# Optimization experiments

Measured on AMD Instinct MI355X. Metric: run time of the kernel, lower is better.

Reference implementation:

```python
import jax, jax.numpy as jnp
import numpy as np

HIDDEN = 128

def setup_inputs() -> dict:
    key = jax.random.key(0)
    k1, k2, k3, k4, k5, k6 = jax.random.split(key, 6)
    n_nodes, n_edges, h = 100000, 500000, HIDDEN
    node_features_after_gcn = jax.random.normal(k1, (n_nodes, h), dtype=jnp.float32)
    edges = jax.random.randint(k2, (2, n_edges), 0, n_nodes, dtype=jnp.int64)
    # edge_classifier params: Linear(2h -> 4h), Linear(4h -> 2)
    W1 = jax.random.normal(k3, (2 * h, 4 * h), dtype=jnp.float32) / np.sqrt(2 * h)
    b1 = jax.random.normal(k4, (4 * h,), dtype=jnp.float32) * 0.01
    W2 = jax.random.normal(k5, (4 * h, 2), dtype=jnp.float32) / np.sqrt(4 * h)
    b2 = jax.random.normal(k6, (2,), dtype=jnp.float32) * 0.01
    return {"node_features_after_gcn": node_features_after_gcn, "edges": edges,
            "W1": W1, "b1": b1, "W2": W2, "b2": b2}

def reference(node_features_after_gcn, W1, b1, W2, b2, edges):
    # gather endpoint features: [E, h] each (node1/node2 projections are Identity)
    first = node_features_after_gcn[edges[0], :]
    second = node_features_after_gcn[edges[1], :]
    edge_feat = jnp.concatenate((first, second), axis=1)  # [E, 2h]
    edge_feat = jax.nn.relu(edge_feat)
    hidden = jax.nn.relu(edge_feat @ W1 + b1)  # [E, 4h]
    return hidden @ W2 + b2  # [E, 2]
```

## Files before the change

### kernel.cpp

```cpp
#include <hip/hip_runtime.h>
#include <stdint.h>

#define HID  128
#define N1   512
#define NCAT 1024
#define NTB  48

typedef _Float16 f16;
typedef __attribute__((ext_vector_type(8))) _Float16 f16x8;
typedef __attribute__((ext_vector_type(4))) _Float16 f16x4;
typedef __attribute__((ext_vector_type(2))) _Float16 f16x2;
typedef __attribute__((ext_vector_type(8))) short   short8;
typedef __attribute__((ext_vector_type(4))) float   floatx4;
typedef __attribute__((ext_vector_type(2))) float   floatx2;
typedef __attribute__((ext_vector_type(8))) __bf16  bf16x8;

static __device__ __forceinline__ short f2bf(float x) {
  uint32_t u = __builtin_bit_cast(uint32_t, x);
  uint32_t r = (u + 0x7FFFu + ((u >> 16) & 1u)) >> 16;
  return (short)r;
}
static __device__ __forceinline__ float bf2f(short s) {
  uint32_t u = ((uint32_t)(uint16_t)s) << 16;
  return __builtin_bit_cast(float, u);
}
static __device__ __forceinline__ f16x2 pkrtz(float a, float b) {
  return __builtin_bit_cast(f16x2, __builtin_amdgcn_cvt_pkrtz(a, b));
}
typedef __fp16 __attribute__((ext_vector_type(2))) fp16v2;
static __device__ __forceinline__ float fdot2(f16x2 a, f16x2 b, float c) {
#if __has_builtin(__builtin_amdgcn_fdot2)
  return __builtin_amdgcn_fdot2(__builtin_bit_cast(fp16v2, a),
                                __builtin_bit_cast(fp16v2, b), c, false);
#else
  return c + (float)a[0] * (float)b[0] + (float)a[1] * (float)b[1];
#endif
}

static __device__ __forceinline__ void gload16(const f16* g, f16* l) {
  __builtin_amdgcn_global_load_lds(
      (const __attribute__((address_space(1))) unsigned int*)g,
      (__attribute__((address_space(3))) unsigned int*)l, 16, 0, 0);
}


__global__ __launch_bounds__(256) void prep_all(
    const float* __restrict__ feats, const float* __restrict__ W1,
    f16* __restrict__ A, f16* __restrict__ BT2, int total4) {
  int idx = blockIdx.x * 256 + threadIdx.x;
  if (idx < total4) {
    floatx4 f = *(const floatx4*)(feats + (size_t)idx * 4);
    f16x4 o;
#pragma unroll
    for (int j = 0; j < 4; ++j) o[j] = (f16)fmaxf(f[j], 0.f);
    *(f16x4*)(A + (size_t)idx * 4) = o;
    return;
  }
  int w = idx - total4;
  if (w < N1 * 256) {
    int n = w >> 8;
    int k = w & 255;
    BT2[w] = (f16)W1[k * N1 + n];
  }
}

#define PIECE(EACC, NN, S0, S1)                                            \
  {                                                                        \
    const int nb_ = n0w + (NN) * 16 + (quad << 2);                         \
    const floatx4 bv_ = *(const floatx4*)&b1s[nb_];                        \
    const f16x4 wq0_ = *(const f16x4*)&w2h0[nb_ >> 1];                     \
    const f16x4 wq1_ = *(const f16x4*)&w2h1[nb_ >> 1];                     \
    floatx2 a01_ = {EACC[NN][0] + bv_[0], EACC[NN][1] + bv_[1]};           \
    floatx2 a23_ = {EACC[NN][2] + bv_[2], EACC[NN][3] + bv_[3]};           \
    a01_ = __builtin_elementwise_max(a01_, (floatx2){0.f, 0.f});           \
    a23_ = __builtin_elementwise_max(a23_, (floatx2){0.f, 0.f});           \
    f16x2 z01_ = pkrtz(a01_[0], a01_[1]);                                  \
    f16x2 z23_ = pkrtz(a23_[0], a23_[1]);                                  \
    S0 = fdot2(z01_, (f16x2){wq0_[0], wq0_[1]}, S0);                       \
    S0 = fdot2(z23_, (f16x2){wq0_[2], wq0_[3]}, S0);                       \
    S1 = fdot2(z01_, (f16x2){wq1_[0], wq1_[1]}, S1);                       \
    S1 = fdot2(z23_, (f16x2){wq1_[2], wq1_[3]}, S1);                       \
  }

#define BURST(MACC, MROW, EPI, EACC, ESLOT, EMT)                           \
  {                                                                        \
    _Pragma("unroll") for (int nn = 0; nn < 4; ++nn)                       \
        MACC[nn] = (floatx4){0.f, 0.f, 0.f, 0.f};                          \
    float es0_ = 0.f, es1_ = 0.f;                                          \
    _Pragma("unroll") for (int kk = 0; kk < 8; ++kk) {                     \
      const f16* base_ = (kk < 4) ? au : av;                               \
      const int coff_ = (((((kk & 3) << 2) + quad)) ^ l16) << 3;           \
      f16x8 af_ = *(const f16x8*)(base_ + ((MROW) * 16 + l16) * HID + coff_); \
      _Pragma("unroll") for (int nn = 0; nn < 4; ++nn)                     \
        MACC[nn] = __builtin_amdgcn_mfma_f32_16x16x32_f16(                 \
            bfr[nn][kk], af_, MACC[nn], 0, 0, 0);                          \
      if (EPI) {                                                           \
        if (kk < 4) { PIECE(EACC, kk, es0_, es1_); }                       \
        else if (kk == 4) { es0_ += __shfl_xor(es0_, 16);                  \
                            es1_ += __shfl_xor(es1_, 16); }                \
        else if (kk == 5) { es0_ += __shfl_xor(es0_, 32);                  \
                            es1_ += __shfl_xor(es1_, 32); }                \
        else if (kk == 6) { if (quad == 0)                                 \
            *(floatx2*)&part[ESLOT][wave][(EMT) * 16 + l16][0] =           \
                (floatx2){es0_, es1_}; }                                   \
      }                                                                    \
    }                                                                      \
  }

__global__ __launch_bounds__(512, 2) void fused_kernel(
    const f16* __restrict__ A,
    const f16* __restrict__ BT2,
    const float* __restrict__ b1,
    const float* __restrict__ W2,
    const float* __restrict__ b2,
    const int* __restrict__ edges,
    float* __restrict__ out,
    int n_edges, int ntiles) {
  __shared__ f16 AU[2][NTB][HID];
  __shared__ f16 AV[2][NTB][HID];
  __shared__ float part[3][8][NTB][2];
  __shared__ float b1s[N1];
  __shared__ f16x2 w2h0[N1 / 2];
  __shared__ f16x2 w2h1[N1 / 2];

  const int tid  = threadIdx.x;
  const int wave = tid >> 6;
  const int lane = tid & 63;
  const int quad = lane >> 4;
  const int l16  = lane & 15;
  const int n0w  = wave << 6;

  if (tid < N1) b1s[tid] = b1[tid];
  if (tid < N1 / 2) {
    floatx4 w = *(const floatx4*)(W2 + 4 * tid);
    w2h0[tid] = pkrtz(w[0], w[2]);
    w2h1[tid] = pkrtz(w[1], w[3]);
  }
  const float b2v0 = b2[0], b2v1 = b2[1];

  f16x8 bfr[4][8];
#pragma unroll
  for (int nn = 0; nn < 4; ++nn) {
    const f16* bp = BT2 + (size_t)(n0w + nn * 16 + l16) * 256 + quad * 8;
#pragma unroll
    for (int kk = 0; kk < 8; ++kk) bfr[nn][kk] = *(const f16x8*)(bp + kk * 32);
  }

  const int j0   = wave * 3;
  const int rsub = lane >> 4;

  int idr[3];
  auto load_idx = [&](int t) {
#pragma unroll
    for (int c = 0; c < 3; ++c) {
      int j = j0 + c;
      int side = (j >= 12) ? 1 : 0;
      int r = ((j - side * 12) << 2) + rsub;
      int e = t * NTB + r;
      if (e >= n_edges) e = n_edges - 1;
      idr[c] = edges[side * n_edges + e];
    }
  };
  auto issue_gather = [&](int b) {
#pragma unroll
    for (int c = 0; c < 3; ++c) {
      int j = j0 + c;
      int side = (j >= 12) ? 1 : 0;
      int r0 = (j - side * 12) << 2;
      int r  = r0 + rsub;
      const f16* src = A + ((size_t)idr[c] << 7) + (((lane & 15) ^ (r & 15)) << 3);
      f16* dst = side ? &AV[b][r0][0] : &AU[b][r0][0];
      gload16(src, dst);
    }
  };

  auto outwrite = [&](int tt, int ps) {
    const int m = tid >> 1, jj = tid & 1;
    float s = part[ps][0][m][jj] + part[ps][1][m][jj] + part[ps][2][m][jj] +
              part[ps][3][m][jj] + part[ps][4][m][jj] + part[ps][5][m][jj] +
              part[ps][6][m][jj] + part[ps][7][m][jj];
    const int e = tt * NTB + m;
    if (e < n_edges) out[2 * (size_t)e + jj] = s + (jj ? b2v1 : b2v0);
  };

  const int NB = gridDim.x;
  const int t0 = blockIdx.x;
  int bb = 0;

  if (t0 < ntiles) {
    load_idx(t0);
    issue_gather(0);
    load_idx(t0 + NB);
  }

  floatx4 acc0[4], acc1[4], acc2[4];

  int i = 0;
  for (int t = t0; t < ntiles; t += NB, ++i) {
    __syncthreads();

    if (t + NB < ntiles) {
      issue_gather(bb ^ 1);
      load_idx(t + 2 * NB);
    }
    if (i >= 2 && tid < 2 * NTB) outwrite(t - 2 * NB, (i - 2) % 3);

    const f16* au = &AU[bb][0][0];
    const f16* av = &AV[bb][0][0];
    const int slotP = (i + 2) % 3;
    const int slotC = i % 3;

    if (i >= 1) {
      BURST(acc0, 0, 1, acc2, slotP, 2);
    } else {
      BURST(acc0, 0, 0, acc0, 0, 0);
    }
    BURST(acc1, 1, 1, acc0, slotC, 0);
    BURST(acc2, 2, 1, acc1, slotC, 1);
    bb ^= 1;
  }

  if (i >= 1) {
    __syncthreads();
    if (i >= 2 && tid < 2 * NTB) outwrite(t0 + (i - 2) * NB, (i - 2) % 3);
    {
      float es0_ = 0.f, es1_ = 0.f;
      PIECE(acc2, 0, es0_, es1_);
      PIECE(acc2, 1, es0_, es1_);
      PIECE(acc2, 2, es0_, es1_);
      PIECE(acc2, 3, es0_, es1_);
      es0_ += __shfl_xor(es0_, 16); es1_ += __shfl_xor(es1_, 16);
      es0_ += __shfl_xor(es0_, 32); es1_ += __shfl_xor(es1_, 32);
      if (quad == 0)
        *(floatx2*)&part[(i + 2) % 3][wave][2 * 16 + l16][0] = (floatx2){es0_, es1_};
    }
    __syncthreads();
    if (tid < 2 * NTB) outwrite(t0 + (i - 1) * NB, (i + 2) % 3);
  }
}


__global__ __launch_bounds__(256) void conv_bt_bf(
    const float* __restrict__ W1, short* __restrict__ BT) {
  int idx = blockIdx.x * 256 + threadIdx.x;
  int n = idx >> 7;
  int k = idx & 127;
  float w = (n < N1) ? W1[k * N1 + n] : W1[(k + HID) * N1 + (n - N1)];
  BT[idx] = f2bf(w);
}

__global__ __launch_bounds__(256) void gemm_bf(
    const float* __restrict__ feats, const short* __restrict__ BT,
    short* __restrict__ GH, int n_nodes) {
  const int wave = threadIdx.x >> 6;
  const int lane = threadIdx.x & 63;
  const int quad = lane >> 4;
  const int l16  = lane & 15;
  const int row0 = blockIdx.x * 64 + wave * 16;
  const int n0   = blockIdx.y * 128;
  const int m  = row0 + l16;
  const int mc = (m < n_nodes) ? m : (n_nodes - 1);
  const float* arow = feats + (size_t)mc * HID;
  floatx4 acc[8];
#pragma unroll
  for (int i = 0; i < 8; ++i) acc[i] = (floatx4){0.f, 0.f, 0.f, 0.f};
#pragma unroll
  for (int kk = 0; kk < 4; ++kk) {
    const int kbase = kk * 32 + quad * 8;
    floatx4 a0 = *(const floatx4*)(arow + kbase);
    floatx4 a1 = *(const floatx4*)(arow + kbase + 4);
    short8 af;
#pragma unroll
    for (int j = 0; j < 4; ++j) { float x = a0[j]; af[j] = f2bf(x > 0.f ? x : 0.f); }
#pragma unroll
    for (int j = 0; j < 4; ++j) { float x = a1[j]; af[4 + j] = f2bf(x > 0.f ? x : 0.f); }
    bf16x8 afrag = __builtin_bit_cast(bf16x8, af);
#pragma unroll
    for (int nn = 0; nn < 8; ++nn) {
      const int n = n0 + nn * 16 + l16;
      short8 bs = *(const short8*)(BT + (size_t)n * HID + kbase);
      acc[nn] = __builtin_amdgcn_mfma_f32_16x16x32_bf16(
          afrag, __builtin_bit_cast(bf16x8, bs), acc[nn], 0, 0, 0);
    }
  }
#pragma unroll
  for (int nn = 0; nn < 8; ++nn) {
    const int col = n0 + nn * 16 + l16;
#pragma unroll
    for (int r = 0; r < 4; ++r) {
      const int row = row0 + quad * 4 + r;
      if (row < n_nodes) GH[(size_t)row * NCAT + col] = f2bf(acc[nn][r]);
    }
  }
}

__global__ __launch_bounds__(256) void edge2_bf(
    const short* __restrict__ GH, const int* __restrict__ edges,
    const float* __restrict__ b1, const float* __restrict__ W2,
    const float* __restrict__ b2, float* __restrict__ out, int n_edges) {
  const int wave = threadIdx.x >> 6;
  const int lane = threadIdx.x & 63;
  const int w = blockIdx.x * 4 + wave;
  const int e0 = 2 * w;
  if (e0 >= n_edges) return;
  const bool has1 = (e0 + 1 < n_edges);
  const int j0 = lane * 8;
  const int u0 = edges[e0];
  const int v0 = edges[n_edges + e0];
  const int u1 = has1 ? edges[e0 + 1] : u0;
  const int v1 = has1 ? edges[n_edges + e0 + 1] : v0;
  short8 g0 = *(const short8*)(GH + (size_t)u0 * NCAT + j0);
  short8 h0 = *(const short8*)(GH + (size_t)v0 * NCAT + N1 + j0);
  short8 g1 = *(const short8*)(GH + (size_t)u1 * NCAT + j0);
  short8 h1 = *(const short8*)(GH + (size_t)v1 * NCAT + N1 + j0);
  float bv[8];
  {
    floatx4 t0 = *(const floatx4*)(b1 + j0);
    floatx4 t1 = *(const floatx4*)(b1 + j0 + 4);
#pragma unroll
    for (int j = 0; j < 4; ++j) { bv[j] = t0[j]; bv[4 + j] = t1[j]; }
  }
  float wv[16];
#pragma unroll
  for (int q = 0; q < 4; ++q) {
    floatx4 tt = *(const floatx4*)(W2 + (size_t)j0 * 2 + q * 4);
#pragma unroll
    for (int j = 0; j < 4; ++j) wv[q * 4 + j] = tt[j];
  }
  float s00 = 0.f, s01 = 0.f, s10 = 0.f, s11 = 0.f;
#pragma unroll
  for (int j = 0; j < 8; ++j) {
    float p0 = bf2f(g0[j]) + bf2f(h0[j]) + bv[j];
    p0 = p0 > 0.f ? p0 : 0.f;
    s00 += p0 * wv[2 * j];
    s01 += p0 * wv[2 * j + 1];
    float p1 = bf2f(g1[j]) + bf2f(h1[j]) + bv[j];
    p1 = p1 > 0.f ? p1 : 0.f;
    s10 += p1 * wv[2 * j];
    s11 += p1 * wv[2 * j + 1];
  }
#pragma unroll
  for (int off = 32; off > 0; off >>= 1) {
    s00 += __shfl_down(s00, off, 64);
    s01 += __shfl_down(s01, off, 64);
    s10 += __shfl_down(s10, off, 64);
    s11 += __shfl_down(s11, off, 64);
  }
  if (lane == 0) {
    out[2 * (size_t)e0]     = s00 + b2[0];
    out[2 * (size_t)e0 + 1] = s01 + b2[1];
    if (has1) {
      out[2 * (size_t)e0 + 2] = s10 + b2[0];
      out[2 * (size_t)e0 + 3] = s11 + b2[1];
    }
  }
}

__global__ __launch_bounds__(256) void slow_kernel(
    const float* __restrict__ feats, const int* __restrict__ edges,
    const float* __restrict__ W1, const float* __restrict__ b1,
    const float* __restrict__ W2, const float* __restrict__ b2,
    float* __restrict__ out, int n_edges) {
  const int wave = threadIdx.x >> 6;
  const int lane = threadIdx.x & 63;
  const int edge = blockIdx.x * 4 + wave;
  if (edge >= n_edges) return;
  const int u = edges[edge];
  const int v = edges[n_edges + edge];
  float f[4];
  f[0] = feats[(size_t)u * HID + lane];
  f[1] = feats[(size_t)u * HID + 64 + lane];
  f[2] = feats[(size_t)v * HID + lane];
  f[3] = feats[(size_t)v * HID + 64 + lane];
#pragma unroll
  for (int i = 0; i < 4; ++i) f[i] = f[i] > 0.f ? f[i] : 0.f;
  const int j0 = lane * 8;
  float acc[8];
#pragma unroll
  for (int j = 0; j < 8; ++j) acc[j] = 0.f;
#pragma unroll
  for (int seg = 0; seg < 4; ++seg) {
    float fs = f[seg];
    for (int k2 = 0; k2 < 64; ++k2) {
      float fk = __shfl(fs, k2, 64);
      const float* wr = W1 + (size_t)(seg * 64 + k2) * N1 + j0;
#pragma unroll
      for (int j = 0; j < 8; ++j) acc[j] += fk * wr[j];
    }
  }
  float s0 = 0.f, s1 = 0.f;
#pragma unroll
  for (int j = 0; j < 8; ++j) {
    float p = acc[j] + b1[j0 + j];
    p = p > 0.f ? p : 0.f;
    s0 += p * W2[(size_t)(j0 + j) * 2];
    s1 += p * W2[(size_t)(j0 + j) * 2 + 1];
  }
#pragma unroll
  for (int off = 32; off > 0; off >>= 1) {
    s0 += __shfl_down(s0, off, 64);
    s1 += __shfl_down(s1, off, 64);
  }
  if (lane == 0) {
    out[2 * (size_t)edge]     = s0 + b2[0];
    out[2 * (size_t)edge + 1] = s1 + b2[1];
  }
}

extern "C" void kernel_launch(void* const* d_in, const int* in_sizes, int n_in,
                              void* d_out, int out_size, void* d_ws, size_t ws_size,
                              hipStream_t stream) {
  const float* feats = (const float*)d_in[0];
  const int*   edges = (const int*)d_in[1];
  const float* W1    = (const float*)d_in[2];
  const float* b1    = (const float*)d_in[3];
  const float* W2    = (const float*)d_in[4];
  const float* b2    = (const float*)d_in[5];
  float* out = (float*)d_out;

  const int n_nodes = in_sizes[0] / HID;
  const int n_edges = in_sizes[1] / 2;

  const size_t bt2_bytes = (size_t)N1 * 256 * 2;
  const size_t a_bytes   = (size_t)n_nodes * HID * 2;

  const size_t bt_bytes = (size_t)NCAT * HID * 2;
  const size_t gh_bytes = (size_t)n_nodes * NCAT * 2;

  if (ws_size >= bt2_bytes + a_bytes) {
    f16* BT2 = (f16*)d_ws;
    f16* A   = (f16*)((char*)d_ws + bt2_bytes);
    const int total4 = n_nodes * (HID / 4);
    const int prep_total = total4 + N1 * 256;
    prep_all<<<(prep_total + 255) / 256, 256, 0, stream>>>(feats, W1, A, BT2, total4);
    const int ntiles = (n_edges + NTB - 1) / NTB;
    const int nb = ntiles < 256 ? ntiles : 256;
    fused_kernel<<<nb, 512, 0, stream>>>(A, BT2, b1, W2, b2, edges, out, n_edges, ntiles);
  } else if (ws_size >= bt_bytes + gh_bytes) {
    short* BT = (short*)d_ws;
    short* GH = (short*)((char*)d_ws + bt_bytes);
    conv_bt_bf<<<(NCAT * HID) / 256, 256, 0, stream>>>(W1, BT);
    dim3 grid((n_nodes + 63) / 64, NCAT / 128);
    gemm_bf<<<grid, 256, 0, stream>>>(feats, BT, GH, n_nodes);
    edge2_bf<<<((n_edges + 1) / 2 + 3) / 4, 256, 0, stream>>>(GH, edges, b1, W2, b2, out, n_edges);
  } else {
    slow_kernel<<<(n_edges + 3) / 4, 256, 0, stream>>>(feats, edges, W1, b1, W2, b2, out, n_edges);
  }
}
```

Measured before the change: 224.5 us.

## Split fused edge MLP across 16 waves and drop software-pipelined epilogue

Doubles the block to 1024 threads (16 waves), so each wave now owns 32 hidden columns instead of 64, which halves the per-wave B-fragment register footprint. The cross-burst software pipeline that interleaved the bias/ReLU/W2 epilogue of one M-tile with the MFMAs of the next is removed. All three M-tiles are now computed first and then reduced, with a simpler double-buffered partial-sum array. The aim is more waves in flight for latency hiding and lower register pressure. In exchange, the epilogue no longer overlaps with MFMA work, the launch bound asks for 4 blocks per CU, and the output reduction now sums 16 partials.

```diff
diff --git a/kernel.cpp b/kernel.cpp
--- a/kernel.cpp
+++ b/kernel.cpp
@@ -5,6 +5,7 @@
 #define N1   512
 #define NCAT 1024
 #define NTB  48
+#define NWAVES 16
 
 typedef _Float16 f16;
 typedef __attribute__((ext_vector_type(8))) _Float16 f16x8;
@@ -64,50 +65,7 @@
   }
 }
 
-#define PIECE(EACC, NN, S0, S1)                                            \
-  {                                                                        \
-    const int nb_ = n0w + (NN) * 16 + (quad << 2);                         \
-    const floatx4 bv_ = *(const floatx4*)&b1s[nb_];                        \
-    const f16x4 wq0_ = *(const f16x4*)&w2h0[nb_ >> 1];                     \
-    const f16x4 wq1_ = *(const f16x4*)&w2h1[nb_ >> 1];                     \
-    floatx2 a01_ = {EACC[NN][0] + bv_[0], EACC[NN][1] + bv_[1]};           \
-    floatx2 a23_ = {EACC[NN][2] + bv_[2], EACC[NN][3] + bv_[3]};           \
-    a01_ = __builtin_elementwise_max(a01_, (floatx2){0.f, 0.f});           \
-    a23_ = __builtin_elementwise_max(a23_, (floatx2){0.f, 0.f});           \
-    f16x2 z01_ = pkrtz(a01_[0], a01_[1]);                                  \
-    f16x2 z23_ = pkrtz(a23_[0], a23_[1]);                                  \
-    S0 = fdot2(z01_, (f16x2){wq0_[0], wq0_[1]}, S0);                       \
-    S0 = fdot2(z23_, (f16x2){wq0_[2], wq0_[3]}, S0);                       \
-    S1 = fdot2(z01_, (f16x2){wq1_[0], wq1_[1]}, S1);                       \
-    S1 = fdot2(z23_, (f16x2){wq1_[2], wq1_[3]}, S1);                       \
-  }
-
-#define BURST(MACC, MROW, EPI, EACC, ESLOT, EMT)                           \
-  {                                                                        \
-    _Pragma("unroll") for (int nn = 0; nn < 4; ++nn)                       \
-        MACC[nn] = (floatx4){0.f, 0.f, 0.f, 0.f};                          \
-    float es0_ = 0.f, es1_ = 0.f;                                          \
-    _Pragma("unroll") for (int kk = 0; kk < 8; ++kk) {                     \
-      const f16* base_ = (kk < 4) ? au : av;                               \
-      const int coff_ = (((((kk & 3) << 2) + quad)) ^ l16) << 3;           \
-      f16x8 af_ = *(const f16x8*)(base_ + ((MROW) * 16 + l16) * HID + coff_); \
-      _Pragma("unroll") for (int nn = 0; nn < 4; ++nn)                     \
-        MACC[nn] = __builtin_amdgcn_mfma_f32_16x16x32_f16(                 \
-            bfr[nn][kk], af_, MACC[nn], 0, 0, 0);                          \
-      if (EPI) {                                                           \
-        if (kk < 4) { PIECE(EACC, kk, es0_, es1_); }                       \
-        else if (kk == 4) { es0_ += __shfl_xor(es0_, 16);                  \
-                            es1_ += __shfl_xor(es1_, 16); }                \
-        else if (kk == 5) { es0_ += __shfl_xor(es0_, 32);                  \
-                            es1_ += __shfl_xor(es1_, 32); }                \
-        else if (kk == 6) { if (quad == 0)                                 \
-            *(floatx2*)&part[ESLOT][wave][(EMT) * 16 + l16][0] =           \
-                (floatx2){es0_, es1_}; }                                   \
-      }                                                                    \
-    }                                                                      \
-  }
-
-__global__ __launch_bounds__(512, 2) void fused_kernel(
+__global__ __launch_bounds__(1024, 4) void fused_kernel(
     const f16* __restrict__ A,
     const f16* __restrict__ BT2,
     const float* __restrict__ b1,
@@ -118,7 +76,7 @@
     int n_edges, int ntiles) {
   __shared__ f16 AU[2][NTB][HID];
   __shared__ f16 AV[2][NTB][HID];
-  __shared__ float part[3][8][NTB][2];
+  __shared__ float part[2][NWAVES][NTB][2];
   __shared__ float b1s[N1];
   __shared__ f16x2 w2h0[N1 / 2];
   __shared__ f16x2 w2h1[N1 / 2];
@@ -128,7 +86,7 @@
   const int lane = tid & 63;
   const int quad = lane >> 4;
   const int l16  = lane & 15;
-  const int n0w  = wave << 6;
+  const int n0w  = wave << 5;
 
   if (tid < N1) b1s[tid] = b1[tid];
   if (tid < N1 / 2) {
@@ -138,47 +96,56 @@
   }
   const float b2v0 = b2[0], b2v1 = b2[1];
 
-  f16x8 bfr[4][8];
-#pragma unroll
-  for (int nn = 0; nn < 4; ++nn) {
+  f16x8 bfr[2][8];
+#pragma unroll
+  for (int nn = 0; nn < 2; ++nn) {
     const f16* bp = BT2 + (size_t)(n0w + nn * 16 + l16) * 256 + quad * 8;
 #pragma unroll
     for (int kk = 0; kk < 8; ++kk) bfr[nn][kk] = *(const f16x8*)(bp + kk * 32);
   }
 
-  const int j0   = wave * 3;
   const int rsub = lane >> 4;
-
-  int idr[3];
+  const int jA = wave;
+  const int jB = 16 + wave;
+  const bool hasB = (wave < 8);
+
+  int idrA, idrB;
   auto load_idx = [&](int t) {
-#pragma unroll
-    for (int c = 0; c < 3; ++c) {
-      int j = j0 + c;
-      int side = (j >= 12) ? 1 : 0;
-      int r = ((j - side * 12) << 2) + rsub;
+    {
+      int side = (jA >= 12) ? 1 : 0;
+      int r = ((jA - side * 12) << 2) + rsub;
       int e = t * NTB + r;
       if (e >= n_edges) e = n_edges - 1;
-      idr[c] = edges[side * n_edges + e];
+      idrA = edges[side * n_edges + e];
+    }
+    if (hasB) {
+      int r = ((jB - 12) << 2) + rsub;
+      int e = t * NTB + r;
+      if (e >= n_edges) e = n_edges - 1;
+      idrB = edges[n_edges + e];
     }
   };
   auto issue_gather = [&](int b) {
-#pragma unroll
-    for (int c = 0; c < 3; ++c) {
-      int j = j0 + c;
-      int side = (j >= 12) ? 1 : 0;
-      int r0 = (j - side * 12) << 2;
+    {
+      int side = (jA >= 12) ? 1 : 0;
+      int r0 = (jA - side * 12) << 2;
       int r  = r0 + rsub;
-      const f16* src = A + ((size_t)idr[c] << 7) + (((lane & 15) ^ (r & 15)) << 3);
-      f16* dst = side ? &AV[b][r0][0] : &AU[b][r0][0];
-      gload16(src, dst);
+      const f16* src = A + ((size_t)idrA << 7) + ((l16 ^ (r & 15)) << 3);
+      gload16(src, side ? &AV[b][r0][0] : &AU[b][r0][0]);
+    }
+    if (hasB) {
+      int r0 = (jB - 12) << 2;
+      int r  = r0 + rsub;
+      const f16* src = A + ((size_t)idrB << 7) + ((l16 ^ (r & 15)) << 3);
+      gload16(src, &AV[b][r0][0]);
     }
   };
 
   auto outwrite = [&](int tt, int ps) {
     const int m = tid >> 1, jj = tid & 1;
-    float s = part[ps][0][m][jj] + part[ps][1][m][jj] + part[ps][2][m][jj] +
-              part[ps][3][m][jj] + part[ps][4][m][jj] + part[ps][5][m][jj] +
-              part[ps][6][m][jj] + part[ps][7][m][jj];
+    float s = 0.f;
+#pragma unroll
+    for (int w = 0; w < NWAVES; ++w) s += part[ps][w][m][jj];
     const int e = tt * NTB + m;
     if (e < n_edges) out[2 * (size_t)e + jj] = s + (jj ? b2v1 : b2v0);
   };
@@ -193,49 +160,68 @@
     load_idx(t0 + NB);
   }
 
-  floatx4 acc0[4], acc1[4], acc2[4];
-
   int i = 0;
-  for (int t = t0; t < ntiles; t += NB, ++i) {
+  int t = t0;
+  for (; t < ntiles; t += NB, ++i) {
     __syncthreads();
 
     if (t + NB < ntiles) {
       issue_gather(bb ^ 1);
       load_idx(t + 2 * NB);
     }
-    if (i >= 2 && tid < 2 * NTB) outwrite(t - 2 * NB, (i - 2) % 3);
+    if (i >= 1 && tid < 2 * NTB) outwrite(t - NB, (i - 1) & 1);
 
     const f16* au = &AU[bb][0][0];
     const f16* av = &AV[bb][0][0];
-    const int slotP = (i + 2) % 3;
-    const int slotC = i % 3;
-
-    if (i >= 1) {
-      BURST(acc0, 0, 1, acc2, slotP, 2);
-    } else {
-      BURST(acc0, 0, 0, acc0, 0, 0);
-    }
-    BURST(acc1, 1, 1, acc0, slotC, 0);
-    BURST(acc2, 2, 1, acc1, slotC, 1);
+    floatx4 acc[3][2];
+#pragma unroll
+    for (int mt = 0; mt < 3; ++mt) {
+      acc[mt][0] = (floatx4){0.f, 0.f, 0.f, 0.f};
+      acc[mt][1] = (floatx4){0.f, 0.f, 0.f, 0.f};
+    }
+#pragma unroll
+    for (int kk = 0; kk < 8; ++kk) {
+      const f16* base = (kk < 4) ? au : av;
+      const int coff = (((((kk & 3) << 2) + quad)) ^ l16) << 3;
+#pragma unroll
+      for (int mt = 0; mt < 3; ++mt) {
+        f16x8 af = *(const f16x8*)(base + (mt * 16 + l16) * HID + coff);
+        acc[mt][0] = __builtin_amdgcn_mfma_f32_16x16x32_f16(bfr[0][kk], af, acc[mt][0], 0, 0, 0);
+        acc[mt][1] = __builtin_amdgcn_mfma_f32_16x16x32_f16(bfr[1][kk], af, acc[mt][1], 0, 0, 0);
+      }
+    }
+
+#pragma unroll
+    for (int mt = 0; mt < 3; ++mt) {
+      float es0 = 0.f, es1 = 0.f;
+#pragma unroll
+      for (int nn = 0; nn < 2; ++nn) {
+        const int nb = n0w + nn * 16 + (quad << 2);
+        const floatx4 bv = *(const floatx4*)&b1s[nb];
+        const f16x4 wq0 = *(const f16x4*)&w2h0[nb >> 1];
+        const f16x4 wq1 = *(const f16x4*)&w2h1[nb >> 1];
+        floatx2 a01 = {acc[mt][nn][0] + bv[0], acc[mt][nn][1] + bv[1]};
+        floatx2 a23 = {acc[mt][nn][2] + bv[2], acc[mt][nn][3] + bv[3]};
+        a01 = __builtin_elementwise_max(a01, (floatx2){0.f, 0.f});
+        a23 = __builtin_elementwise_max(a23, (floatx2){0.f, 0.f});
+        f16x2 z01 = pkrtz(a01[0], a01[1]);
+        f16x2 z23 = pkrtz(a23[0], a23[1]);
+        es0 = fdot2(z01, (f16x2){wq0[0], wq0[1]}, es0);
+        es0 = fdot2(z23, (f16x2){wq0[2], wq0[3]}, es0);
+        es1 = fdot2(z01, (f16x2){wq1[0], wq1[1]}, es1);
+        es1 = fdot2(z23, (f16x2){wq1[2], wq1[3]}, es1);
+      }
+      es0 += __shfl_xor(es0, 16); es1 += __shfl_xor(es1, 16);
+      es0 += __shfl_xor(es0, 32); es1 += __shfl_xor(es1, 32);
+      if (quad == 0)
+        *(floatx2*)&part[i & 1][wave][mt * 16 + l16][0] = (floatx2){es0, es1};
+    }
     bb ^= 1;
   }
 
   if (i >= 1) {
     __syncthreads();
-    if (i >= 2 && tid < 2 * NTB) outwrite(t0 + (i - 2) * NB, (i - 2) % 3);
-    {
-      float es0_ = 0.f, es1_ = 0.f;
-      PIECE(acc2, 0, es0_, es1_);
-      PIECE(acc2, 1, es0_, es1_);
-      PIECE(acc2, 2, es0_, es1_);
-      PIECE(acc2, 3, es0_, es1_);
-      es0_ += __shfl_xor(es0_, 16); es1_ += __shfl_xor(es1_, 16);
-      es0_ += __shfl_xor(es0_, 32); es1_ += __shfl_xor(es1_, 32);
-      if (quad == 0)
-        *(floatx2*)&part[(i + 2) % 3][wave][2 * 16 + l16][0] = (floatx2){es0_, es1_};
-    }
-    __syncthreads();
-    if (tid < 2 * NTB) outwrite(t0 + (i - 1) * NB, (i + 2) % 3);
+    if (tid < 2 * NTB) outwrite(t0 + (i - 1) * NB, (i - 1) & 1);
   }
 }
 
@@ -435,7 +421,7 @@
     prep_all<<<(prep_total + 255) / 256, 256, 0, stream>>>(feats, W1, A, BT2, total4);
     const int ntiles = (n_edges + NTB - 1) / NTB;
     const int nb = ntiles < 256 ? ntiles : 256;
-    fused_kernel<<<nb, 512, 0, stream>>>(A, BT2, b1, W2, b2, edges, out, n_edges, ntiles);
+    fused_kernel<<<nb, 1024, 0, stream>>>(A, BT2, b1, W2, b2, edges, out, n_edges, ntiles);
   } else if (ws_size >= bt_bytes + gh_bytes) {
     short* BT = (short*)d_ws;
     short* GH = (short*)((char*)d_ws + bt_bytes);
```

Measured after the change: 242.9 us. 8.2% more time.
